# Kernel optimization log

Measured on AMD Instinct MI355X. Metric: run time of the kernel, lower is better.

Reference implementation:

```python
import jax, jax.numpy as jnp
import numpy as np

D = 2048          # hidden_size
E = 32            # num_experts
DFF = 1024        # moe_intermediate_size
T = 1024          # tokens (batch*seq)
TOP_K = 4         # num_experts_per_token
N_GROUP = 4
TOPK_GROUP = 2
SCALING = 2.5     # routed_scaling_factor
N_SHARED = 1
SHARED_DFF = DFF * N_SHARED


def setup_inputs() -> dict:
    key = jax.random.key(0)
    ks = jax.random.split(key, 9)
    def init(k, shape, fan_in):
        return jax.random.normal(k, shape, jnp.float32) * (fan_in ** -0.5)
    return {
        "x": jax.random.normal(ks[0], (T, D), jnp.float32),
        "gate_w": init(ks[1], (E, D), D),                 # router Linear weight [out,in]
        "bias": jnp.zeros((E,), jnp.float32),             # e_score_correction_bias
        "Wg": init(ks[2], (E, DFF, D), D),                # expert gate_proj
        "Wu": init(ks[3], (E, DFF, D), D),                # expert up_proj
        "Wd": init(ks[4], (E, D, DFF), DFF),              # expert down_proj
        "sWg": init(ks[5], (SHARED_DFF, D), D),           # shared expert
        "sWu": init(ks[6], (SHARED_DFF, D), D),
        "sWd": init(ks[7], (D, SHARED_DFF), SHARED_DFF),
    }


def _group_expert_select(gates, bias):
    # gates: [T, E]
    scores = jax.nn.sigmoid(gates)            # score_function='sigmoid'
    orig = scores
    scores = scores + bias
    Eg = E // N_GROUP
    s = scores.reshape(-1, N_GROUP, Eg)       # [T, G, Eg]
    group_scores = jax.lax.top_k(s, 2)[0].sum(-1)          # [T, G] sum of top-2 per group
    k = N_GROUP - TOPK_GROUP
    gidx = jax.lax.top_k(group_scores, k)[1]               # [T, k] largest-scoring groups
    # faithful to torch scatter_ with index shape [...,k,1]: only column 0 of
    # the selected groups is marked True; everything else is zeroed.
    mask = jnp.zeros(s.shape, bool)
    t_idx = jnp.arange(s.shape[0])[:, None]
    mask = mask.at[t_idx, gidx, 0].set(True)
    s = jnp.where(mask, s, 0.0)
    scores = s.reshape(-1, E)
    inds = jax.lax.top_k(scores, TOP_K)[1]                 # [T, K]
    w = jnp.take_along_axis(orig, inds, axis=-1)           # gather original scores
    # top_k > 1 and renormalize
    w = w / (w.sum(-1, keepdims=True) + 1e-20)
    return inds, w * SCALING


def _routed_experts(x, inds, w, Wg, Wu, Wd):
    # Combine dispatch + weighted sum: out[t] = sum_k w[t,k] * expert_{inds[t,k]}(x[t]).
    # Equivalently accumulate coeff[t,e] * expert_e(x[t]) with a scan over experts
    # (fixed structural loop over E weight matrices, vectorized over tokens).
    Tn = x.shape[0]
    coeff = jnp.zeros((Tn, E), x.dtype).at[jnp.arange(Tn)[:, None], inds].add(w)  # [T, E]

    def step(acc, we):
        wg, wu, wd, c = we                      # [DFF,D], [DFF,D], [D,DFF], [T]
        h = jax.nn.silu(x @ wg.T) * (x @ wu.T)  # swiglu: [T, DFF]
        return acc + c[:, None] * (h @ wd.T), None

    out, _ = jax.lax.scan(step, jnp.zeros_like(x), (Wg, Wu, Wd, coeff.T))
    return out


def reference(x, gate_w, bias, Wg, Wu, Wd, sWg, sWu, sWd):
    gates = x @ gate_w.T                                   # [T, E]
    inds, w = _group_expert_select(gates, bias)
    out = _routed_experts(x, inds, w, Wg, Wu, Wd)
    shared = (jax.nn.silu(x @ sWg.T) * (x @ sWu.T)) @ sWd.T
    return out + shared
```

## Files before the change

### kernel.cpp

```cpp
#include <hip/hip_runtime.h>
#include <hip/hip_bf16.h>
#include <math.h>

#define DIM  2048
#define NEXP 32
#define DFF  1024
#define NTOK 1024
#define TOPK 4
#define NGRP 4
#define EPG  8
#define SCALE 2.5f

#define BM 128
#define BN 64
#define BK 64
#define MAX_TILES 80
#define MAX_ROWS  10240

typedef unsigned int  uint_t;
typedef unsigned short us_t;

typedef __attribute__((ext_vector_type(8))) short bf16x8;
typedef __attribute__((ext_vector_type(4))) float f32x4;

__device__ inline us_t f2b(float f) {
  __hip_bfloat16 h = __float2bfloat16(f);
  return *reinterpret_cast<const us_t*>(&h);
}

__device__ inline uint4 cvt8(float4 a, float4 b) {
  uint4 r;
  r.x = (uint_t)f2b(a.x) | ((uint_t)f2b(a.y) << 16);
  r.y = (uint_t)f2b(a.z) | ((uint_t)f2b(a.w) << 16);
  r.z = (uint_t)f2b(b.x) | ((uint_t)f2b(b.y) << 16);
  r.w = (uint_t)f2b(b.z) | ((uint_t)f2b(b.w) << 16);
  return r;
}

__global__ __launch_bounds__(256) void xcast_kernel(const float4* __restrict__ x4,
                                                    uint2* __restrict__ xb4) {
  int i = blockIdx.x * 256 + threadIdx.x;
  float4 v = x4[i];
  uint2 o;
  o.x = (uint_t)f2b(v.x) | ((uint_t)f2b(v.y) << 16);
  o.y = (uint_t)f2b(v.z) | ((uint_t)f2b(v.w) << 16);
  xb4[i] = o;
}

__global__ __launch_bounds__(64) void router_kernel(const float* __restrict__ x,
                                                    const float* __restrict__ gw,
                                                    const float* __restrict__ bias,
                                                    int* __restrict__ inds,
                                                    float* __restrict__ wts) {
  int t = blockIdx.x, l = threadIdx.x;
  float xr[32];
#pragma unroll
  for (int i = 0; i < 32; i++) xr[i] = x[t * DIM + i * 64 + l];
  __shared__ float lg[NEXP];
  for (int e = 0; e < NEXP; e++) {
    const float* w = gw + e * DIM;
    float acc = 0.f;
#pragma unroll
    for (int i = 0; i < 32; i++) acc += xr[i] * w[i * 64 + l];
#pragma unroll
    for (int off = 32; off > 0; off >>= 1) acc += __shfl_xor(acc, off);
    if (l == 0) lg[e] = acc;
  }
  __syncthreads();
  if (l != 0) return;

  float s[NEXP], sb[NEXP], mv[NEXP];
#pragma unroll
  for (int e = 0; e < NEXP; e++) {
    float sv = 1.f / (1.f + expf(-lg[e]));
    s[e] = sv; sb[e] = sv + bias[e];
  }
  float gs[NGRP];
#pragma unroll
  for (int g = 0; g < NGRP; g++) {
    float m1 = -1e30f, m2 = -1e30f;
#pragma unroll
    for (int j = 0; j < EPG; j++) {
      float v = sb[g * EPG + j];
      if (v > m1) { m2 = m1; m1 = v; } else if (v > m2) { m2 = v; }
    }
    gs[g] = m1 + m2;
  }
  int g1 = 0;
#pragma unroll
  for (int g = 1; g < NGRP; g++) if (gs[g] > gs[g1]) g1 = g;
  int g2 = -1; float g2v = -1e30f;
#pragma unroll
  for (int g = 0; g < NGRP; g++) {
    if (g == g1) continue;
    if (gs[g] > g2v) { g2v = gs[g]; g2 = g; }
  }
#pragma unroll
  for (int e = 0; e < NEXP; e++) {
    bool keep = (e == g1 * EPG) || (e == g2 * EPG);
    mv[e] = keep ? sb[e] : 0.f;
  }
  uint_t used = 0; float wsum = 0.f;
  int id[TOPK]; float wv[TOPK];
#pragma unroll
  for (int kk = 0; kk < TOPK; kk++) {
    float bv = -1e30f, bs = 0.f; int best = 0;
#pragma unroll
    for (int e = 0; e < NEXP; e++) {
      bool ok = !((used >> e) & 1u) && (mv[e] > bv);
      if (ok) { bv = mv[e]; best = e; bs = s[e]; }
    }
    used |= (1u << best);
    id[kk] = best; wv[kk] = bs; wsum += bs;
  }
  float inv = SCALE / (wsum + 1e-20f);
#pragma unroll
  for (int kk = 0; kk < TOPK; kk++) {
    inds[t * TOPK + kk] = id[kk];
    wts[t * TOPK + kk] = wv[kk] * inv;
  }
}

__global__ __launch_bounds__(256) void plan_kernel(const int* __restrict__ inds,
                                                   const float* __restrict__ wts,
                                                   int* __restrict__ row2tok,
                                                   float* __restrict__ roww,
                                                   int* __restrict__ tileE,
                                                   int* __restrict__ tileR,
                                                   int* __restrict__ nT) {
  __shared__ int wsum[4];
  __shared__ int s_off, s_nt;
  int tid = threadIdx.x, lane = tid & 63, wv = tid >> 6;
  if (tid == 0) { s_off = 0; s_nt = 0; }
  __syncthreads();
  for (int e = 0; e < NEXP; e++) {
    int off0 = s_off;
    int slot[4]; int cnt = 0;
    int tb = tid * 4;
#pragma unroll
    for (int j = 0; j < 4; j++) {
      int t = tb + j; int sl = -1;
#pragma unroll
      for (int k = 0; k < TOPK; k++) if (inds[t * TOPK + k] == e) sl = k;
      slot[j] = sl; cnt += (sl >= 0) ? 1 : 0;
    }
    int v = cnt;
#pragma unroll
    for (int off = 1; off < 64; off <<= 1) {
      int u = __shfl_up(v, (unsigned)off);
      if (lane >= off) v += u;
    }
    if (lane == 63) wsum[wv] = v;
    __syncthreads();
    int base = 0;
#pragma unroll
    for (int w = 0; w < 4; w++) base += (w < wv) ? wsum[w] : 0;
    int total = wsum[0] + wsum[1] + wsum[2] + wsum[3];
    int r = off0 + base + v - cnt;
#pragma unroll
    for (int j = 0; j < 4; j++) {
      if (slot[j] >= 0) {
        int t = tb + j;
        row2tok[r] = t; roww[r] = wts[t * TOPK + slot[j]];
        r++;
      }
    }
    int ntm = (total + BM - 1) / BM;
    int padEnd = off0 + ntm * BM;
    for (int q = off0 + total + tid; q < padEnd; q += 256) { row2tok[q] = 0; roww[q] = 0.f; }
    __syncthreads();
    if (tid == 0) {
      for (int i = 0; i < ntm; i++) { tileE[s_nt + i] = e; tileR[s_nt + i] = off0 + i * BM; }
      s_nt += ntm; s_off = padEnd;
    }
    __syncthreads();
  }
  int off0 = s_off;
  for (int t = tid; t < NTOK; t += 256) { row2tok[off0 + t] = t; roww[off0 + t] = 1.f; }
  if (tid == 0) {
    for (int i = 0; i < NTOK / BM; i++) { tileE[s_nt + i] = NEXP; tileR[s_nt + i] = off0 + i * BM; }
    nT[0] = s_nt + NTOK / BM;
  }
}

__global__ __launch_bounds__(512) void gateup_kernel(const us_t* __restrict__ xb,
                                                     const float* __restrict__ Wg,
                                                     const float* __restrict__ Wu,
                                                     const float* __restrict__ sWg,
                                                     const float* __restrict__ sWu,
                                                     const int* __restrict__ row2tok,
                                                     const int* __restrict__ tileE,
                                                     const int* __restrict__ tileR,
                                                     const int* __restrict__ nT,
                                                     us_t* __restrict__ H) {
  int hw = blockIdx.x;
  int work = (hw & 7) * (MAX_TILES * (DFF / BN) / 8) + (hw >> 3);
  int tile = work % MAX_TILES;
  int n0 = (work / MAX_TILES) * BN;
  if (tile >= nT[0]) return;
  int e = tileE[tile], row0 = tileR[tile];
  const float* wgp = (e < NEXP) ? (Wg + (size_t)e * DFF * DIM) : sWg;
  const float* wup = (e < NEXP) ? (Wu + (size_t)e * DFF * DIM) : sWu;

  __shared__ us_t Xs[BM][BK];
  __shared__ us_t Gs[BN][BK];
  __shared__ us_t Us[BN][BK];

  int tid = threadIdx.x;
  int lane = tid & 63;
  int wid = tid >> 6;
  int wm = (wid >> 1) * 32, wn = (wid & 1) * 32;

  int srow = tid >> 2;
  int c0 = (tid & 3) * 2;
  int scol = (tid & 3) * 16;
  int sw = srow & 7;
  int tok = row2tok[row0 + srow];
  const us_t* xrow = xb + (size_t)tok * DIM;
  int wr = tid >> 3;
  int wc = tid & 7;
  int wsw = wc ^ (wr & 7);
  const float* grow = wgp + (size_t)(n0 + wr) * DIM + wc * 8;
  const float* urow = wup + (size_t)(n0 + wr) * DIM + wc * 8;

  f32x4 accg[2][2] = {};
  f32x4 accu[2][2] = {};

  for (int kt = 0; kt < DIM; kt += BK) {
    {
      const uint4* src = (const uint4*)(xrow + kt + scol);
      uint4 a = src[0], b = src[1];
      uint4* dst = (uint4*)&Xs[srow][0];
      dst[c0 ^ sw] = a; dst[(c0 + 1) ^ sw] = b;
    }
    {
      const float4* s4 = (const float4*)(grow + kt);
      float4 a = s4[0], b = s4[1];
      ((uint4*)&Gs[wr][0])[wsw] = cvt8(a, b);
    }
    {
      const float4* s4 = (const float4*)(urow + kt);
      float4 a = s4[0], b = s4[1];
      ((uint4*)&Us[wr][0])[wsw] = cvt8(a, b);
    }
    __syncthreads();
#pragma unroll
    for (int ks = 0; ks < BK; ks += 32) {
      int cb = (ks >> 3) + (lane >> 4);
      bf16x8 af[2], bg[2], bu[2];
#pragma unroll
      for (int mi = 0; mi < 2; mi++) {
        int r = wm + mi * 16 + (lane & 15);
        af[mi] = *(const bf16x8*)&(((const uint4*)&Xs[r][0])[cb ^ (r & 7)]);
      }
#pragma unroll
      for (int ni = 0; ni < 2; ni++) {
        int r = wn + ni * 16 + (lane & 15);
        bg[ni] = *(const bf16x8*)&(((const uint4*)&Gs[r][0])[cb ^ (r & 7)]);
        bu[ni] = *(const bf16x8*)&(((const uint4*)&Us[r][0])[cb ^ (r & 7)]);
      }
#pragma unroll
      for (int mi = 0; mi < 2; mi++)
#pragma unroll
        for (int ni = 0; ni < 2; ni++) {
          accg[mi][ni] = __builtin_amdgcn_mfma_f32_16x16x32_bf16(af[mi], bg[ni], accg[mi][ni], 0, 0, 0);
          accu[mi][ni] = __builtin_amdgcn_mfma_f32_16x16x32_bf16(af[mi], bu[ni], accu[mi][ni], 0, 0, 0);
        }
    }
    __syncthreads();
  }
#pragma unroll
  for (int mi = 0; mi < 2; mi++) {
#pragma unroll
    for (int j = 0; j < 4; j++) {
      int r = row0 + wm + mi * 16 + (lane >> 4) * 4 + j;
      us_t* hrow = H + (size_t)r * DFF;
#pragma unroll
      for (int ni = 0; ni < 2; ni++) {
        float g = accg[mi][ni][j], u = accu[mi][ni][j];
        float h = (g / (1.f + expf(-g))) * u;
        hrow[n0 + wn + ni * 16 + (lane & 15)] = f2b(h);
      }
    }
  }
}

__global__ __launch_bounds__(512) void down_kernel(const us_t* __restrict__ H,
                                                   const float* __restrict__ Wd,
                                                   const float* __restrict__ sWd,
                                                   const int* __restrict__ row2tok,
                                                   const float* __restrict__ roww,
                                                   const int* __restrict__ tileE,
                                                   const int* __restrict__ tileR,
                                                   const int* __restrict__ nT,
                                                   float* __restrict__ out) {
  int hw = blockIdx.x;
  int work = (hw & 7) * (MAX_TILES * (DIM / BN) / 8) + (hw >> 3);
  int tile = work % MAX_TILES;
  int n0 = (work / MAX_TILES) * BN;
  if (tile >= nT[0]) return;
  int e = tileE[tile], row0 = tileR[tile];
  const float* wd = (e < NEXP) ? (Wd + (size_t)e * DIM * DFF) : sWd;

  __shared__ us_t Hs[BM][BK];
  __shared__ us_t Ds[BN][BK];

  int tid = threadIdx.x;
  int lane = tid & 63;
  int wid = tid >> 6;
  int wm = (wid >> 1) * 32, wn = (wid & 1) * 32;

  int srow = tid >> 2;
  int c0 = (tid & 3) * 2;
  int scol = (tid & 3) * 16;
  int sw = srow & 7;
  const us_t* hrow = H + (size_t)(row0 + srow) * DFF;
  int wr = tid >> 3;
  int wc = tid & 7;
  int wsw = wc ^ (wr & 7);
  const float* drow = wd + (size_t)(n0 + wr) * DFF + wc * 8;

  f32x4 acc[2][2] = {};

  for (int kt = 0; kt < DFF; kt += BK) {
    {
      const uint4* src = (const uint4*)(hrow + kt + scol);
      uint4 a = src[0], b = src[1];
      uint4* dst = (uint4*)&Hs[srow][0];
      dst[c0 ^ sw] = a; dst[(c0 + 1) ^ sw] = b;
    }
    {
      const float4* s4 = (const float4*)(drow + kt);
      float4 a = s4[0], b = s4[1];
      ((uint4*)&Ds[wr][0])[wsw] = cvt8(a, b);
    }
    __syncthreads();
#pragma unroll
    for (int ks = 0; ks < BK; ks += 32) {
      int cb = (ks >> 3) + (lane >> 4);
      bf16x8 af[2], bw[2];
#pragma unroll
      for (int mi = 0; mi < 2; mi++) {
        int r = wm + mi * 16 + (lane & 15);
        af[mi] = *(const bf16x8*)&(((const uint4*)&Hs[r][0])[cb ^ (r & 7)]);
      }
#pragma unroll
      for (int ni = 0; ni < 2; ni++) {
        int r = wn + ni * 16 + (lane & 15);
        bw[ni] = *(const bf16x8*)&(((const uint4*)&Ds[r][0])[cb ^ (r & 7)]);
      }
#pragma unroll
      for (int mi = 0; mi < 2; mi++)
#pragma unroll
        for (int ni = 0; ni < 2; ni++)
          acc[mi][ni] = __builtin_amdgcn_mfma_f32_16x16x32_bf16(af[mi], bw[ni], acc[mi][ni], 0, 0, 0);
    }
    __syncthreads();
  }
#pragma unroll
  for (int mi = 0; mi < 2; mi++) {
#pragma unroll
    for (int j = 0; j < 4; j++) {
      int r = row0 + wm + mi * 16 + (lane >> 4) * 4 + j;
      float wgt = roww[r];
      int tok = row2tok[r];
      float* orow = out + (size_t)tok * DIM;
#pragma unroll
      for (int ni = 0; ni < 2; ni++)
        atomicAdd(orow + n0 + wn + ni * 16 + (lane & 15), acc[mi][ni][j] * wgt);
    }
  }
}

extern "C" void kernel_launch(void* const* d_in, const int* in_sizes, int n_in,
                              void* d_out, int out_size, void* d_ws, size_t ws_size,
                              hipStream_t stream) {
  const float* x    = (const float*)d_in[0];
  const float* gw   = (const float*)d_in[1];
  const float* bias = (const float*)d_in[2];
  const float* Wg   = (const float*)d_in[3];
  const float* Wu   = (const float*)d_in[4];
  const float* Wd   = (const float*)d_in[5];
  const float* sWg  = (const float*)d_in[6];
  const float* sWu  = (const float*)d_in[7];
  const float* sWd  = (const float*)d_in[8];
  float* out = (float*)d_out;

  char* p = (char*)d_ws;
  us_t* xb = (us_t*)p;            p += (size_t)NTOK * DIM * 2;
  us_t* H  = (us_t*)p;            p += (size_t)MAX_ROWS * DFF * 2;
  int* inds = (int*)p;            p += NTOK * TOPK * 4;
  float* wts = (float*)p;         p += NTOK * TOPK * 4;
  int* row2tok = (int*)p;         p += MAX_ROWS * 4;
  float* roww = (float*)p;        p += MAX_ROWS * 4;
  int* tileE = (int*)p;           p += MAX_TILES * 4;
  int* tileR = (int*)p;           p += MAX_TILES * 4;
  int* nT = (int*)p;              p += 4;

  hipMemsetAsync(d_out, 0, (size_t)NTOK * DIM * 4, stream);
  hipLaunchKernelGGL(xcast_kernel, dim3(NTOK * DIM / 1024), dim3(256), 0, stream,
                     (const float4*)x, (uint2*)xb);
  hipLaunchKernelGGL(router_kernel, dim3(NTOK), dim3(64), 0, stream, x, gw, bias, inds, wts);
  hipLaunchKernelGGL(plan_kernel, dim3(1), dim3(256), 0, stream,
                     inds, wts, row2tok, roww, tileE, tileR, nT);
  hipLaunchKernelGGL(gateup_kernel, dim3(MAX_TILES * (DFF / BN)), dim3(512), 0, stream,
                     xb, Wg, Wu, sWg, sWu, row2tok, tileE, tileR, nT, H);
  hipLaunchKernelGGL(down_kernel, dim3(MAX_TILES * (DIM / BN)), dim3(512), 0, stream,
                     H, Wd, sWd, row2tok, roww, tileE, tileR, nT, out);
}
```

Baseline: 258.7 us.

## Prefetch next K-tile into registers in GEMM kernels, fuse output zeroing

```diff
diff --git a/kernel.cpp b/kernel.cpp
--- a/kernel.cpp
+++ b/kernel.cpp
@@ -23,6 +23,9 @@
 typedef __attribute__((ext_vector_type(8))) short bf16x8;
 typedef __attribute__((ext_vector_type(4))) float f32x4;
 
+#define BARSYNC() do { asm volatile("s_waitcnt lgkmcnt(0)" ::: "memory"); \
+                       __builtin_amdgcn_s_barrier(); } while (0)
+
 __device__ inline us_t f2b(float f) {
   __hip_bfloat16 h = __float2bfloat16(f);
   return *reinterpret_cast<const us_t*>(&h);
@@ -38,13 +41,15 @@
 }
 
 __global__ __launch_bounds__(256) void xcast_kernel(const float4* __restrict__ x4,
-                                                    uint2* __restrict__ xb4) {
+                                                    uint2* __restrict__ xb4,
+                                                    float4* __restrict__ out4) {
   int i = blockIdx.x * 256 + threadIdx.x;
   float4 v = x4[i];
   uint2 o;
   o.x = (uint_t)f2b(v.x) | ((uint_t)f2b(v.y) << 16);
   o.y = (uint_t)f2b(v.z) | ((uint_t)f2b(v.w) << 16);
   xb4[i] = o;
+  out4[i] = make_float4(0.f, 0.f, 0.f, 0.f);
 }
 
 __global__ __launch_bounds__(64) void router_kernel(const float* __restrict__ x,
@@ -132,16 +137,21 @@
   __shared__ int s_off, s_nt;
   int tid = threadIdx.x, lane = tid & 63, wv = tid >> 6;
   if (tid == 0) { s_off = 0; s_nt = 0; }
+  int tb = tid * 4;
+  int myi[16];
+#pragma unroll
+  for (int j = 0; j < 4; j++)
+#pragma unroll
+    for (int k = 0; k < TOPK; k++) myi[j * 4 + k] = inds[(tb + j) * TOPK + k];
   __syncthreads();
   for (int e = 0; e < NEXP; e++) {
     int off0 = s_off;
     int slot[4]; int cnt = 0;
-    int tb = tid * 4;
 #pragma unroll
     for (int j = 0; j < 4; j++) {
-      int t = tb + j; int sl = -1;
-#pragma unroll
-      for (int k = 0; k < TOPK; k++) if (inds[t * TOPK + k] == e) sl = k;
+      int sl = -1;
+#pragma unroll
+      for (int k = 0; k < TOPK; k++) if (myi[j * 4 + k] == e) sl = k;
       slot[j] = sl; cnt += (sl >= 0) ? 1 : 0;
     }
     int v = cnt;
@@ -226,24 +236,26 @@
   f32x4 accg[2][2] = {};
   f32x4 accu[2][2] = {};
 
-  for (int kt = 0; kt < DIM; kt += BK) {
-    {
-      const uint4* src = (const uint4*)(xrow + kt + scol);
-      uint4 a = src[0], b = src[1];
-      uint4* dst = (uint4*)&Xs[srow][0];
-      dst[c0 ^ sw] = a; dst[(c0 + 1) ^ sw] = b;
-    }
-    {
-      const float4* s4 = (const float4*)(grow + kt);
-      float4 a = s4[0], b = s4[1];
-      ((uint4*)&Gs[wr][0])[wsw] = cvt8(a, b);
-    }
-    {
-      const float4* s4 = (const float4*)(urow + kt);
-      float4 a = s4[0], b = s4[1];
-      ((uint4*)&Us[wr][0])[wsw] = cvt8(a, b);
-    }
-    __syncthreads();
+  uint4 xr0, xr1; float4 gr0, gr1, ur0, ur1;
+  uint4 xn0, xn1; float4 gn0, gn1, un0, un1;
+
+#define GU_LOAD(KT, X0, X1, G0, G1, U0, U1) do {              \
+    const uint4* xs_ = (const uint4*)(xrow + (KT) + scol);    \
+    X0 = xs_[0]; X1 = xs_[1];                                 \
+    const float4* gs_ = (const float4*)(grow + (KT));         \
+    G0 = gs_[0]; G1 = gs_[1];                                 \
+    const float4* us_ = (const float4*)(urow + (KT));         \
+    U0 = us_[0]; U1 = us_[1];                                 \
+  } while (0)
+
+#define GU_STAGE(X0, X1, G0, G1, U0, U1) do {                 \
+    uint4* dx_ = (uint4*)&Xs[srow][0];                        \
+    dx_[c0 ^ sw] = X0; dx_[(c0 + 1) ^ sw] = X1;               \
+    ((uint4*)&Gs[wr][0])[wsw] = cvt8(G0, G1);                 \
+    ((uint4*)&Us[wr][0])[wsw] = cvt8(U0, U1);                 \
+  } while (0)
+
+  auto compute = [&]() {
 #pragma unroll
     for (int ks = 0; ks < BK; ks += 32) {
       int cb = (ks >> 3) + (lane >> 4);
@@ -267,8 +279,22 @@
           accu[mi][ni] = __builtin_amdgcn_mfma_f32_16x16x32_bf16(af[mi], bu[ni], accu[mi][ni], 0, 0, 0);
         }
     }
-    __syncthreads();
-  }
+  };
+
+  GU_LOAD(0, xr0, xr1, gr0, gr1, ur0, ur1);
+  for (int kt = 0; kt < DIM; kt += 2 * BK) {
+    GU_LOAD(kt + BK, xn0, xn1, gn0, gn1, un0, un1);
+    GU_STAGE(xr0, xr1, gr0, gr1, ur0, ur1);
+    BARSYNC();
+    compute();
+    BARSYNC();
+    if (kt + 2 * BK < DIM) GU_LOAD(kt + 2 * BK, xr0, xr1, gr0, gr1, ur0, ur1);
+    GU_STAGE(xn0, xn1, gn0, gn1, un0, un1);
+    BARSYNC();
+    compute();
+    BARSYNC();
+  }
+
 #pragma unroll
   for (int mi = 0; mi < 2; mi++) {
 #pragma unroll
@@ -322,19 +348,23 @@
 
   f32x4 acc[2][2] = {};
 
-  for (int kt = 0; kt < DFF; kt += BK) {
-    {
-      const uint4* src = (const uint4*)(hrow + kt + scol);
-      uint4 a = src[0], b = src[1];
-      uint4* dst = (uint4*)&Hs[srow][0];
-      dst[c0 ^ sw] = a; dst[(c0 + 1) ^ sw] = b;
-    }
-    {
-      const float4* s4 = (const float4*)(drow + kt);
-      float4 a = s4[0], b = s4[1];
-      ((uint4*)&Ds[wr][0])[wsw] = cvt8(a, b);
-    }
-    __syncthreads();
+  uint4 hr0, hr1; float4 dr0, dr1;
+  uint4 hn0, hn1; float4 dn0, dn1;
+
+#define DN_LOAD(KT, H0, H1, D0, D1) do {                      \
+    const uint4* hs_ = (const uint4*)(hrow + (KT) + scol);    \
+    H0 = hs_[0]; H1 = hs_[1];                                 \
+    const float4* ds_ = (const float4*)(drow + (KT));         \
+    D0 = ds_[0]; D1 = ds_[1];                                 \
+  } while (0)
+
+#define DN_STAGE(H0, H1, D0, D1) do {                         \
+    uint4* dh_ = (uint4*)&Hs[srow][0];                        \
+    dh_[c0 ^ sw] = H0; dh_[(c0 + 1) ^ sw] = H1;               \
+    ((uint4*)&Ds[wr][0])[wsw] = cvt8(D0, D1);                 \
+  } while (0)
+
+  auto compute = [&]() {
 #pragma unroll
     for (int ks = 0; ks < BK; ks += 32) {
       int cb = (ks >> 3) + (lane >> 4);
@@ -355,8 +385,22 @@
         for (int ni = 0; ni < 2; ni++)
           acc[mi][ni] = __builtin_amdgcn_mfma_f32_16x16x32_bf16(af[mi], bw[ni], acc[mi][ni], 0, 0, 0);
     }
-    __syncthreads();
-  }
+  };
+
+  DN_LOAD(0, hr0, hr1, dr0, dr1);
+  for (int kt = 0; kt < DFF; kt += 2 * BK) {
+    DN_LOAD(kt + BK, hn0, hn1, dn0, dn1);
+    DN_STAGE(hr0, hr1, dr0, dr1);
+    BARSYNC();
+    compute();
+    BARSYNC();
+    if (kt + 2 * BK < DFF) DN_LOAD(kt + 2 * BK, hr0, hr1, dr0, dr1);
+    DN_STAGE(hn0, hn1, dn0, dn1);
+    BARSYNC();
+    compute();
+    BARSYNC();
+  }
+
 #pragma unroll
   for (int mi = 0; mi < 2; mi++) {
 #pragma unroll
@@ -397,9 +441,8 @@
   int* tileR = (int*)p;           p += MAX_TILES * 4;
   int* nT = (int*)p;              p += 4;
 
-  hipMemsetAsync(d_out, 0, (size_t)NTOK * DIM * 4, stream);
   hipLaunchKernelGGL(xcast_kernel, dim3(NTOK * DIM / 1024), dim3(256), 0, stream,
-                     (const float4*)x, (uint2*)xb);
+                     (const float4*)x, (uint2*)xb, (float4*)out);
   hipLaunchKernelGGL(router_kernel, dim3(NTOK), dim3(64), 0, stream, x, gw, bias, inds, wts);
   hipLaunchKernelGGL(plan_kernel, dim3(1), dim3(256), 0, stream,
                      inds, wts, row2tok, roww, tileE, tileR, nT);
```

Measured after the change: 280.6 us. 8.5% more time.

## Widen GEMM tiles to 128x128, use direct global-to-LDS loads, fuse output zeroing

Applied to the files above, without the earlier changes.

```diff
diff --git a/kernel.cpp b/kernel.cpp
--- a/kernel.cpp
+++ b/kernel.cpp
@@ -12,7 +12,7 @@
 #define SCALE 2.5f
 
 #define BM 128
-#define BN 64
+#define BN 128
 #define BK 64
 #define MAX_TILES 80
 #define MAX_ROWS  10240
@@ -22,6 +22,10 @@
 
 typedef __attribute__((ext_vector_type(8))) short bf16x8;
 typedef __attribute__((ext_vector_type(4))) float f32x4;
+
+#define GLOAD_LDS16(g, l) __builtin_amdgcn_global_load_lds( \
+    (const __attribute__((address_space(1))) unsigned int*)(g), \
+    (__attribute__((address_space(3))) unsigned int*)(l), 16, 0, 0)
 
 __device__ inline us_t f2b(float f) {
   __hip_bfloat16 h = __float2bfloat16(f);
@@ -38,13 +42,15 @@
 }
 
 __global__ __launch_bounds__(256) void xcast_kernel(const float4* __restrict__ x4,
-                                                    uint2* __restrict__ xb4) {
+                                                    uint2* __restrict__ xb4,
+                                                    float4* __restrict__ out4) {
   int i = blockIdx.x * 256 + threadIdx.x;
   float4 v = x4[i];
   uint2 o;
   o.x = (uint_t)f2b(v.x) | ((uint_t)f2b(v.y) << 16);
   o.y = (uint_t)f2b(v.z) | ((uint_t)f2b(v.w) << 16);
   xb4[i] = o;
+  out4[i] = make_float4(0.f, 0.f, 0.f, 0.f);
 }
 
 __global__ __launch_bounds__(64) void router_kernel(const float* __restrict__ x,
@@ -132,16 +138,21 @@
   __shared__ int s_off, s_nt;
   int tid = threadIdx.x, lane = tid & 63, wv = tid >> 6;
   if (tid == 0) { s_off = 0; s_nt = 0; }
+  int tb = tid * 4;
+  int myi[16];
+#pragma unroll
+  for (int j = 0; j < 4; j++)
+#pragma unroll
+    for (int k = 0; k < TOPK; k++) myi[j * 4 + k] = inds[(tb + j) * TOPK + k];
   __syncthreads();
   for (int e = 0; e < NEXP; e++) {
     int off0 = s_off;
     int slot[4]; int cnt = 0;
-    int tb = tid * 4;
 #pragma unroll
     for (int j = 0; j < 4; j++) {
-      int t = tb + j; int sl = -1;
-#pragma unroll
-      for (int k = 0; k < TOPK; k++) if (inds[t * TOPK + k] == e) sl = k;
+      int sl = -1;
+#pragma unroll
+      for (int k = 0; k < TOPK; k++) if (myi[j * 4 + k] == e) sl = k;
       slot[j] = sl; cnt += (sl >= 0) ? 1 : 0;
     }
     int v = cnt;
@@ -209,58 +220,59 @@
   int tid = threadIdx.x;
   int lane = tid & 63;
   int wid = tid >> 6;
-  int wm = (wid >> 1) * 32, wn = (wid & 1) * 32;
-
-  int srow = tid >> 2;
-  int c0 = (tid & 3) * 2;
-  int scol = (tid & 3) * 16;
-  int sw = srow & 7;
-  int tok = row2tok[row0 + srow];
-  const us_t* xrow = xb + (size_t)tok * DIM;
-  int wr = tid >> 3;
-  int wc = tid & 7;
-  int wsw = wc ^ (wr & 7);
-  const float* grow = wgp + (size_t)(n0 + wr) * DIM + wc * 8;
-  const float* urow = wup + (size_t)(n0 + wr) * DIM + wc * 8;
-
-  f32x4 accg[2][2] = {};
-  f32x4 accu[2][2] = {};
+  int wmr = (wid >> 2) * 64;
+  int wnc = (wid & 3) * 32;
+
+  int s0 = wid * 128 + lane, s1 = s0 + 64;
+  int xr0 = s0 >> 3, xc0 = s0 & 7;
+  int xr1 = s1 >> 3, xc1 = s1 & 7;
+  const us_t* xsrc0 = xb + (size_t)row2tok[row0 + xr0] * DIM + (xc0 ^ (xr0 & 7)) * 8;
+  const us_t* xsrc1 = xb + (size_t)row2tok[row0 + xr1] * DIM + (xc1 ^ (xr1 & 7)) * 8;
+  us_t* xdst0 = &Xs[0][0] + (size_t)(wid * 128) * 8;
+  us_t* xdst1 = xdst0 + 64 * 8;
+
+  int a0 = tid, a1 = tid + 512;
+  int ar0 = a0 >> 3, ac0 = a0 & 7;
+  int ar1 = a1 >> 3, ac1 = a1 & 7;
+  const float* gsrc0 = wgp + (size_t)(n0 + ar0) * DIM + (ac0 ^ (ar0 & 7)) * 8;
+  const float* gsrc1 = wgp + (size_t)(n0 + ar1) * DIM + (ac1 ^ (ar1 & 7)) * 8;
+  const float* usrc0 = wup + (size_t)(n0 + ar0) * DIM + (ac0 ^ (ar0 & 7)) * 8;
+  const float* usrc1 = wup + (size_t)(n0 + ar1) * DIM + (ac1 ^ (ar1 & 7)) * 8;
+  uint4* gdst0 = (uint4*)((char*)&Gs[0][0] + (size_t)a0 * 16);
+  uint4* gdst1 = (uint4*)((char*)&Gs[0][0] + (size_t)a1 * 16);
+  uint4* udst0 = (uint4*)((char*)&Us[0][0] + (size_t)a0 * 16);
+  uint4* udst1 = (uint4*)((char*)&Us[0][0] + (size_t)a1 * 16);
+
+  f32x4 accg[4][2] = {};
+  f32x4 accu[4][2] = {};
 
   for (int kt = 0; kt < DIM; kt += BK) {
+    GLOAD_LDS16(xsrc0 + kt, xdst0);
+    GLOAD_LDS16(xsrc1 + kt, xdst1);
     {
-      const uint4* src = (const uint4*)(xrow + kt + scol);
-      uint4 a = src[0], b = src[1];
-      uint4* dst = (uint4*)&Xs[srow][0];
-      dst[c0 ^ sw] = a; dst[(c0 + 1) ^ sw] = b;
-    }
-    {
-      const float4* s4 = (const float4*)(grow + kt);
-      float4 a = s4[0], b = s4[1];
-      ((uint4*)&Gs[wr][0])[wsw] = cvt8(a, b);
-    }
-    {
-      const float4* s4 = (const float4*)(urow + kt);
-      float4 a = s4[0], b = s4[1];
-      ((uint4*)&Us[wr][0])[wsw] = cvt8(a, b);
+      const float4* p = (const float4*)(gsrc0 + kt); *gdst0 = cvt8(p[0], p[1]);
+      p = (const float4*)(gsrc1 + kt);               *gdst1 = cvt8(p[0], p[1]);
+      p = (const float4*)(usrc0 + kt);               *udst0 = cvt8(p[0], p[1]);
+      p = (const float4*)(usrc1 + kt);               *udst1 = cvt8(p[0], p[1]);
     }
     __syncthreads();
 #pragma unroll
     for (int ks = 0; ks < BK; ks += 32) {
       int cb = (ks >> 3) + (lane >> 4);
-      bf16x8 af[2], bg[2], bu[2];
-#pragma unroll
-      for (int mi = 0; mi < 2; mi++) {
-        int r = wm + mi * 16 + (lane & 15);
+      bf16x8 af[4], bg[2], bu[2];
+#pragma unroll
+      for (int mi = 0; mi < 4; mi++) {
+        int r = wmr + mi * 16 + (lane & 15);
         af[mi] = *(const bf16x8*)&(((const uint4*)&Xs[r][0])[cb ^ (r & 7)]);
       }
 #pragma unroll
       for (int ni = 0; ni < 2; ni++) {
-        int r = wn + ni * 16 + (lane & 15);
+        int r = wnc + ni * 16 + (lane & 15);
         bg[ni] = *(const bf16x8*)&(((const uint4*)&Gs[r][0])[cb ^ (r & 7)]);
         bu[ni] = *(const bf16x8*)&(((const uint4*)&Us[r][0])[cb ^ (r & 7)]);
       }
 #pragma unroll
-      for (int mi = 0; mi < 2; mi++)
+      for (int mi = 0; mi < 4; mi++)
 #pragma unroll
         for (int ni = 0; ni < 2; ni++) {
           accg[mi][ni] = __builtin_amdgcn_mfma_f32_16x16x32_bf16(af[mi], bg[ni], accg[mi][ni], 0, 0, 0);
@@ -270,16 +282,16 @@
     __syncthreads();
   }
 #pragma unroll
-  for (int mi = 0; mi < 2; mi++) {
+  for (int mi = 0; mi < 4; mi++) {
 #pragma unroll
     for (int j = 0; j < 4; j++) {
-      int r = row0 + wm + mi * 16 + (lane >> 4) * 4 + j;
+      int r = row0 + wmr + mi * 16 + (lane >> 4) * 4 + j;
       us_t* hrow = H + (size_t)r * DFF;
 #pragma unroll
       for (int ni = 0; ni < 2; ni++) {
         float g = accg[mi][ni][j], u = accu[mi][ni][j];
         float h = (g / (1.f + expf(-g))) * u;
-        hrow[n0 + wn + ni * 16 + (lane & 15)] = f2b(h);
+        hrow[n0 + wnc + ni * 16 + (lane & 15)] = f2b(h);
       }
     }
   }
@@ -308,49 +320,51 @@
   int tid = threadIdx.x;
   int lane = tid & 63;
   int wid = tid >> 6;
-  int wm = (wid >> 1) * 32, wn = (wid & 1) * 32;
-
-  int srow = tid >> 2;
-  int c0 = (tid & 3) * 2;
-  int scol = (tid & 3) * 16;
-  int sw = srow & 7;
-  const us_t* hrow = H + (size_t)(row0 + srow) * DFF;
-  int wr = tid >> 3;
-  int wc = tid & 7;
-  int wsw = wc ^ (wr & 7);
-  const float* drow = wd + (size_t)(n0 + wr) * DFF + wc * 8;
-
-  f32x4 acc[2][2] = {};
+  int wmr = (wid >> 2) * 64;
+  int wnc = (wid & 3) * 32;
+
+  int s0 = wid * 128 + lane, s1 = s0 + 64;
+  int hr0 = s0 >> 3, hc0 = s0 & 7;
+  int hr1 = s1 >> 3, hc1 = s1 & 7;
+  const us_t* hsrc0 = H + (size_t)(row0 + hr0) * DFF + (hc0 ^ (hr0 & 7)) * 8;
+  const us_t* hsrc1 = H + (size_t)(row0 + hr1) * DFF + (hc1 ^ (hr1 & 7)) * 8;
+  us_t* hdst0 = &Hs[0][0] + (size_t)(wid * 128) * 8;
+  us_t* hdst1 = hdst0 + 64 * 8;
+
+  int a0 = tid, a1 = tid + 512;
+  int ar0 = a0 >> 3, ac0 = a0 & 7;
+  int ar1 = a1 >> 3, ac1 = a1 & 7;
+  const float* dsrc0 = wd + (size_t)(n0 + ar0) * DFF + (ac0 ^ (ar0 & 7)) * 8;
+  const float* dsrc1 = wd + (size_t)(n0 + ar1) * DFF + (ac1 ^ (ar1 & 7)) * 8;
+  uint4* ddst0 = (uint4*)((char*)&Ds[0][0] + (size_t)a0 * 16);
+  uint4* ddst1 = (uint4*)((char*)&Ds[0][0] + (size_t)a1 * 16);
+
+  f32x4 acc[4][2] = {};
 
   for (int kt = 0; kt < DFF; kt += BK) {
+    GLOAD_LDS16(hsrc0 + kt, hdst0);
+    GLOAD_LDS16(hsrc1 + kt, hdst1);
     {
-      const uint4* src = (const uint4*)(hrow + kt + scol);
-      uint4 a = src[0], b = src[1];
-      uint4* dst = (uint4*)&Hs[srow][0];
-      dst[c0 ^ sw] = a; dst[(c0 + 1) ^ sw] = b;
-    }
-    {
-      const float4* s4 = (const float4*)(drow + kt);
-      float4 a = s4[0], b = s4[1];
-      ((uint4*)&Ds[wr][0])[wsw] = cvt8(a, b);
+      const float4* p = (const float4*)(dsrc0 + kt); *ddst0 = cvt8(p[0], p[1]);
+      p = (const float4*)(dsrc1 + kt);               *ddst1 = cvt8(p[0], p[1]);
     }
     __syncthreads();
 #pragma unroll
     for (int ks = 0; ks < BK; ks += 32) {
       int cb = (ks >> 3) + (lane >> 4);
-      bf16x8 af[2], bw[2];
-#pragma unroll
-      for (int mi = 0; mi < 2; mi++) {
-        int r = wm + mi * 16 + (lane & 15);
+      bf16x8 af[4], bw[2];
+#pragma unroll
+      for (int mi = 0; mi < 4; mi++) {
+        int r = wmr + mi * 16 + (lane & 15);
         af[mi] = *(const bf16x8*)&(((const uint4*)&Hs[r][0])[cb ^ (r & 7)]);
       }
 #pragma unroll
       for (int ni = 0; ni < 2; ni++) {
-        int r = wn + ni * 16 + (lane & 15);
+        int r = wnc + ni * 16 + (lane & 15);
         bw[ni] = *(const bf16x8*)&(((const uint4*)&Ds[r][0])[cb ^ (r & 7)]);
       }
 #pragma unroll
-      for (int mi = 0; mi < 2; mi++)
+      for (int mi = 0; mi < 4; mi++)
 #pragma unroll
         for (int ni = 0; ni < 2; ni++)
           acc[mi][ni] = __builtin_amdgcn_mfma_f32_16x16x32_bf16(af[mi], bw[ni], acc[mi][ni], 0, 0, 0);
@@ -358,16 +372,16 @@
     __syncthreads();
   }
 #pragma unroll
-  for (int mi = 0; mi < 2; mi++) {
+  for (int mi = 0; mi < 4; mi++) {
 #pragma unroll
     for (int j = 0; j < 4; j++) {
-      int r = row0 + wm + mi * 16 + (lane >> 4) * 4 + j;
+      int r = row0 + wmr + mi * 16 + (lane >> 4) * 4 + j;
       float wgt = roww[r];
       int tok = row2tok[r];
       float* orow = out + (size_t)tok * DIM;
 #pragma unroll
       for (int ni = 0; ni < 2; ni++)
-        atomicAdd(orow + n0 + wn + ni * 16 + (lane & 15), acc[mi][ni][j] * wgt);
+        atomicAdd(orow + n0 + wnc + ni * 16 + (lane & 15), acc[mi][ni][j] * wgt);
     }
   }
 }
@@ -397,9 +411,8 @@
   int* tileR = (int*)p;           p += MAX_TILES * 4;
   int* nT = (int*)p;              p += 4;
 
-  hipMemsetAsync(d_out, 0, (size_t)NTOK * DIM * 4, stream);
   hipLaunchKernelGGL(xcast_kernel, dim3(NTOK * DIM / 1024), dim3(256), 0, stream,
-                     (const float4*)x, (uint2*)xb);
+                     (const float4*)x, (uint2*)xb, (float4*)out);
   hipLaunchKernelGGL(router_kernel, dim3(NTOK), dim3(64), 0, stream, x, gw, bias, inds, wts);
   hipLaunchKernelGGL(plan_kernel, dim3(1), dim3(256), 0, stream,
                      inds, wts, row2tok, roww, tileE, tileR, nT);
```

Measured after the change: 244.1 us. 1.06x faster.
